# Kernel tuning notes

Hardware: AMD Instinct MI355X
Metric: run time of the kernel (lower is better)

## Reference

```python
import jax, jax.numpy as jnp
import numpy as np

N = 131072          # collocation points
NT, NX = 4, 8       # subdomain grid: 4 time segments x 8 space segments
S = NT * NX         # 32 subdomains
D = 2               # (t, x)
H = 32              # hidden width
OVERLAP = 0.3


def _make_subdomains():
    # t in [0,1] split into NT, x in [-1,1] split into NX
    t_edges = np.linspace(0.0, 1.0, NT + 1)
    x_edges = np.linspace(-1.0, 1.0, NX + 1)
    centers, widths, cmin, cmax = [], [], [], []
    for i in range(NT):
        for j in range(NX):
            lo = np.array([t_edges[i], x_edges[j]])
            hi = np.array([t_edges[i + 1], x_edges[j + 1]])
            centers.append((lo + hi) / 2)
            widths.append(hi - lo)
            cmin.append(lo)
            cmax.append(hi)
    f32 = lambda a: jnp.asarray(np.stack(a), dtype=jnp.float32)
    return f32(centers), f32(widths), f32(cmin), f32(cmax)


def setup_inputs() -> dict:
    key = jax.random.key(0)
    ks = jax.random.split(key, 12)
    # collocation points: t ~ U[0,1], x ~ U[-1,1]
    u = jax.random.uniform(ks[0], (N, D), dtype=jnp.float32)
    X = jnp.stack([u[:, 0], 2.0 * u[:, 1] - 1.0], axis=-1)
    centers, widths, core_min, core_max = _make_subdomains()
    overlap = jnp.full((S, D), OVERLAP, dtype=jnp.float32)
    g = lambda k, sh, fan: (jax.random.normal(k, sh, dtype=jnp.float32)
                            / np.sqrt(fan).astype(np.float32))
    return {
        "X": X,
        "centers": centers, "widths": widths,
        "core_min": core_min, "core_max": core_max, "overlap": overlap,
        "W1": g(ks[1], (S, D, H), D), "b1": jnp.zeros((S, H), jnp.float32),
        "W2": g(ks[2], (S, H, H), H), "b2": jnp.zeros((S, H), jnp.float32),
        "W3": g(ks[3], (S, H, H), H), "b3": jnp.zeros((S, H), jnp.float32),
        "Wout": g(ks[4], (S, H, 1), H), "bout": jnp.zeros((S, 1), jnp.float32),
        "scale": jnp.ones((1,), jnp.float32), "shift": jnp.zeros((1,), jnp.float32),
    }


def reference(X, centers, widths, core_min, core_max, overlap,
              W1, b1, W2, b2, W3, b3, Wout, bout, scale, shift):
    # --- window weights, all subdomains at once: (S, N) ---
    s = 4.0 / (2.0 * overlap * widths + 1e-8)            # (S, D)
    left = jax.nn.sigmoid(s[:, None] * (X[None] - core_min[:, None]))   # (S,N,D)
    right = jax.nn.sigmoid(s[:, None] * (core_max[:, None] - X[None]))  # (S,N,D)
    w = (left * right).prod(axis=-1)                     # (S, N)
    w = w / (w.sum(axis=0, keepdims=True) + 1e-8)

    # --- per-subdomain normalization + batched 3-hidden-layer tanh MLP ---
    xn = (X[None] - centers[:, None]) / widths[:, None] + 0.5           # (S,N,D)
    h = jnp.tanh(jnp.einsum('snd,sdh->snh', xn, W1) + b1[:, None])
    h = jnp.tanh(jnp.einsum('snh,shk->snk', h, W2) + b2[:, None])
    h = jnp.tanh(jnp.einsum('snh,shk->snk', h, W3) + b3[:, None])
    y = jnp.einsum('snh,sho->sno', h, Wout) + bout[:, None]             # (S,N,1)
    y = scale * y + shift                                # shared Unnorm

    out = jnp.sum(w[..., None] * y, axis=0)              # (N, 1)

    # --- hard BC constraint layer ---
    x = X[:, 1]
    t = X[:, 0]
    factor = jnp.tanh(x + 1.0) * jnp.tanh(x - 1.0) * jnp.tanh(t)
    out = -jnp.sin(jnp.pi * x)[:, None] + factor[:, None] * out
    return out
```

## Files before the change

### kernel.cpp

```cpp
#include <hip/hip_runtime.h>
#include <math.h>

typedef short    bf16x8 __attribute__((ext_vector_type(8)));
typedef float    f32x16 __attribute__((ext_vector_type(16)));
typedef float    f32x4  __attribute__((ext_vector_type(4)));
typedef unsigned int u32x4 __attribute__((ext_vector_type(4)));

#define SWZ(row) ((((row) >> 1) & 3) << 3)

__device__ __forceinline__ unsigned short f2bf(float f) {
    unsigned int u = __builtin_bit_cast(unsigned int, f);
    u = (u + 0x7FFFu + ((u >> 16) & 1u)) >> 16;
    return (unsigned short)u;
}
__device__ __forceinline__ unsigned int cvt_pk_bf16(float lo, float hi) {
    unsigned int r;
    asm("v_cvt_pk_bf16_f32 %0, %1, %2" : "=v"(r) : "v"(lo), "v"(hi));
    return r;
}
__device__ __forceinline__ float rcp_fast(float x) { return __builtin_amdgcn_rcpf(x); }

__device__ __forceinline__ float tanh_f(float z) {
    return fmaf(-2.0f, rcp_fast(__expf(2.0f * z) + 1.0f), 1.0f);
}
__device__ __forceinline__ unsigned int sx32(unsigned int v) {
    return (unsigned int)__shfl_xor((int)v, 32, 64);
}

__global__ __launch_bounds__(256) void fbpinn_main(
    const float* __restrict__ X,
    const float* __restrict__ centers,
    const float* __restrict__ widths,
    const float* __restrict__ core_min,
    const float* __restrict__ core_max,
    const float* __restrict__ overlap,
    const float* __restrict__ W1,
    const float* __restrict__ b1,
    const float* __restrict__ W2,
    const float* __restrict__ b2,
    const float* __restrict__ W3,
    const float* __restrict__ b3,
    const float* __restrict__ Wout,
    const float* __restrict__ bout,
    float* __restrict__ ws,
    int n_pts, int s_count)
{
    __shared__ __align__(16) unsigned short sW2t[4][1024];
    __shared__ __align__(16) unsigned short sW3t[4][1024];
    __shared__ __align__(16) float sW1f[4][64];
    __shared__ __align__(16) float sB1[4][32], sB2[4][32], sB3[4][32], sWo[4][32];
    __shared__ float sBout[4];

    const int tid  = threadIdx.x;
    const int wave = tid >> 6;
    const int lane = tid & 63;
    const int p    = lane & 31;
    const int hi   = lane >> 5;
    const int s_begin = blockIdx.y * s_count;

    int P = blockIdx.x * 128 + wave * 32 + p;
    if (P >= n_pts) P = n_pts - 1;

    const float t = X[2 * P + 0];
    const float x = X[2 * P + 1];

    float num = 0.0f, den = 0.0f;

    const int ef0 = (p << 5) + ((hi * 8)      ^ SWZ(p));
    const int ef1 = (p << 5) + ((16 + hi * 8) ^ SWZ(p));

    for (int c0 = 0; c0 < s_count; c0 += 4) {
        __syncthreads();
        {
            const float* W2s = W2 + (size_t)(s_begin + c0) * 1024;
            const float* W3s = W3 + (size_t)(s_begin + c0) * 1024;
            #pragma unroll
            for (int i = 0; i < 16; ++i) {
                int e = tid + (i << 8);
                int sl = e >> 10, r = e & 1023;
                int k = r >> 5, j = r & 31;
                int di = (j << 5) + (k ^ SWZ(j));
                sW2t[sl][di] = f2bf(W2s[e]);
                sW3t[sl][di] = f2bf(W3s[e]);
            }
            sW1f[tid >> 6][tid & 63] = W1[(size_t)(s_begin + c0) * 64 + tid];
            if (tid < 128) {
                int sl = tid >> 5, j = tid & 31;
                int g = (s_begin + c0 + sl) * 32 + j;
                sB1[sl][j] = b1[g];
                sB2[sl][j] = b2[g];
                sB3[sl][j] = b3[g];
                sWo[sl][j] = Wout[g];
            }
            if (tid < 4) sBout[tid] = bout[s_begin + c0 + tid];
        }
        __syncthreads();

        for (int si = 0; si < 4; ++si) {
            const int s = s_begin + c0 + si;

            float wid0 = widths[s * 2 + 0], wid1 = widths[s * 2 + 1];
            float sd0 = 4.0f * rcp_fast(fmaf(2.0f * overlap[s * 2 + 0], wid0, 1e-8f));
            float sd1 = 4.0f * rcp_fast(fmaf(2.0f * overlap[s * 2 + 1], wid1, 1e-8f));
            float z0 = sd0 * (t - core_min[s * 2 + 0]);
            float z1 = sd0 * (core_max[s * 2 + 0] - t);
            float z2 = sd1 * (x - core_min[s * 2 + 1]);
            float z3 = sd1 * (core_max[s * 2 + 1] - x);
            float w = rcp_fast(((1.0f + __expf(-z0)) * (1.0f + __expf(-z1)))
                             * ((1.0f + __expf(-z2)) * (1.0f + __expf(-z3))));
            float xn0 = (t - centers[s * 2 + 0]) * rcp_fast(wid0) + 0.5f;
            float xn1 = (x - centers[s * 2 + 1]) * rcp_fast(wid1) + 0.5f;

            unsigned int pk[8];

            {
                const f32x4* Wa4 = (const f32x4*)&sW1f[si][hi * 16];
                const f32x4* Wb4 = (const f32x4*)&sW1f[si][32 + hi * 16];
                const f32x4* Bv4 = (const f32x4*)&sB1[si][hi * 16];
                float Wa[16], Wb[16], Bv[16];
                #pragma unroll
                for (int i = 0; i < 4; ++i) {
                    f32x4 av = Wa4[i], bv = Wb4[i], cv = Bv4[i];
                    #pragma unroll
                    for (int q = 0; q < 4; ++q) {
                        Wa[4 * i + q] = av[q];
                        Wb[4 * i + q] = bv[q];
                        Bv[4 * i + q] = cv[q];
                    }
                }
                #pragma unroll
                for (int q = 0; q < 8; ++q) {
                    float a0 = fmaf(xn0, Wa[2 * q],     fmaf(xn1, Wb[2 * q],     Bv[2 * q]));
                    float a1 = fmaf(xn0, Wa[2 * q + 1], fmaf(xn1, Wb[2 * q + 1], Bv[2 * q + 1]));
                    pk[q] = cvt_pk_bf16(tanh_f(a0), tanh_f(a1));
                }
            }
            bf16x8 Bf0, Bf1;
            {
                unsigned int r0 = sx32(hi ? pk[0] : pk[4]);
                unsigned int r1 = sx32(hi ? pk[1] : pk[5]);
                unsigned int r2 = sx32(hi ? pk[2] : pk[6]);
                unsigned int r3 = sx32(hi ? pk[3] : pk[7]);
                u32x4 f1 = hi ? (u32x4){r0, r1, r2, r3} : (u32x4){pk[0], pk[1], pk[2], pk[3]};
                u32x4 f2 = hi ? (u32x4){pk[4], pk[5], pk[6], pk[7]} : (u32x4){r0, r1, r2, r3};
                Bf0 = __builtin_bit_cast(bf16x8, f1);
                Bf1 = __builtin_bit_cast(bf16x8, f2);
            }

            f32x16 acc;
            {
                bf16x8 A0 = *(bf16x8*)&sW2t[si][ef0];
                bf16x8 A1 = *(bf16x8*)&sW2t[si][ef1];
                #pragma unroll
                for (int i = 0; i < 4; ++i) {
                    f32x4 bv = *(const f32x4*)&sB2[si][8 * i + 4 * hi];
                    #pragma unroll
                    for (int q = 0; q < 4; ++q) acc[4 * i + q] = bv[q];
                }
                acc = __builtin_amdgcn_mfma_f32_32x32x16_bf16(A0, Bf0, acc, 0, 0, 0);
                acc = __builtin_amdgcn_mfma_f32_32x32x16_bf16(A1, Bf1, acc, 0, 0, 0);
            }
            #pragma unroll
            for (int q = 0; q < 8; ++q)
                pk[q] = cvt_pk_bf16(tanh_f(acc[2 * q]), tanh_f(acc[2 * q + 1]));
            {
                unsigned int r0 = sx32(hi ? pk[0] : pk[2]);
                unsigned int r1 = sx32(hi ? pk[1] : pk[3]);
                unsigned int r2 = sx32(hi ? pk[4] : pk[6]);
                unsigned int r3 = sx32(hi ? pk[5] : pk[7]);
                u32x4 f1 = hi ? (u32x4){r0, r1, pk[2], pk[3]} : (u32x4){pk[0], pk[1], r0, r1};
                u32x4 f2 = hi ? (u32x4){r2, r3, pk[6], pk[7]} : (u32x4){pk[4], pk[5], r2, r3};
                Bf0 = __builtin_bit_cast(bf16x8, f1);
                Bf1 = __builtin_bit_cast(bf16x8, f2);
            }

            {
                bf16x8 A0 = *(bf16x8*)&sW3t[si][ef0];
                bf16x8 A1 = *(bf16x8*)&sW3t[si][ef1];
                #pragma unroll
                for (int i = 0; i < 4; ++i) {
                    f32x4 bv = *(const f32x4*)&sB3[si][8 * i + 4 * hi];
                    #pragma unroll
                    for (int q = 0; q < 4; ++q) acc[4 * i + q] = bv[q];
                }
                acc = __builtin_amdgcn_mfma_f32_32x32x16_bf16(A0, Bf0, acc, 0, 0, 0);
                acc = __builtin_amdgcn_mfma_f32_32x32x16_bf16(A1, Bf1, acc, 0, 0, 0);
            }

            {
                float yp = 0.0f;
                #pragma unroll
                for (int i = 0; i < 4; ++i) {
                    f32x4 wv = *(const f32x4*)&sWo[si][8 * i + 4 * hi];
                    #pragma unroll
                    for (int q = 0; q < 4; ++q)
                        yp = fmaf(tanh_f(acc[4 * i + q]), wv[q], yp);
                }
                float y = yp + __shfl_xor(yp, 32, 64);
                y += sBout[si];
                num = fmaf(w, y, num);
                den += w;
            }
        }
    }

    if (hi == 0) {
        const int grp = blockIdx.y;
        ws[(size_t)(2 * grp)     * n_pts + P] = num;
        ws[(size_t)(2 * grp + 1) * n_pts + P] = den;
    }
}

__global__ __launch_bounds__(256) void fbpinn_combine(
    const float* __restrict__ X,
    const float* __restrict__ scale,
    const float* __restrict__ shift,
    const float* __restrict__ ws,
    float* __restrict__ out,
    int n_pts, int ngrp)
{
    const int P = blockIdx.x * 256 + threadIdx.x;
    if (P >= n_pts) return;
    float num = 0.0f, den = 0.0f;
    for (int g = 0; g < ngrp; ++g) {
        num += ws[(size_t)(2 * g)     * n_pts + P];
        den += ws[(size_t)(2 * g + 1) * n_pts + P];
    }
    const float sc = scale[0], sh = shift[0];
    float u = fmaf(sc, num, sh * den) / (den + 1e-8f);
    const float t = X[2 * P + 0];
    const float x = X[2 * P + 1];
    float fac = tanh_f(x + 1.0f) * tanh_f(x - 1.0f) * tanh_f(t);
    const float pi = 3.14159265358979323846f;
    out[P] = fmaf(fac, u, -__sinf(pi * x));
}

extern "C" void kernel_launch(void* const* d_in, const int* in_sizes, int n_in,
                              void* d_out, int out_size, void* d_ws, size_t ws_size,
                              hipStream_t stream) {
    const float* X        = (const float*)d_in[0];
    const float* centers  = (const float*)d_in[1];
    const float* widths   = (const float*)d_in[2];
    const float* core_min = (const float*)d_in[3];
    const float* core_max = (const float*)d_in[4];
    const float* overlap  = (const float*)d_in[5];
    const float* W1       = (const float*)d_in[6];
    const float* b1       = (const float*)d_in[7];
    const float* W2       = (const float*)d_in[8];
    const float* b2       = (const float*)d_in[9];
    const float* W3       = (const float*)d_in[10];
    const float* b3       = (const float*)d_in[11];
    const float* Wout     = (const float*)d_in[12];
    const float* bout     = (const float*)d_in[13];
    const float* scale    = (const float*)d_in[14];
    const float* shift    = (const float*)d_in[15];

    float* out = (float*)d_out;
    float* ws  = (float*)d_ws;
    const int n_pts = in_sizes[0] / 2;

    int ngrp = 8;
    while (ngrp > 1 && (size_t)2 * ngrp * n_pts * sizeof(float) > ws_size) ngrp >>= 1;
    const int s_count = 32 / ngrp;

    dim3 grid((n_pts + 127) / 128, ngrp);
    fbpinn_main<<<grid, 256, 0, stream>>>(
        X, centers, widths, core_min, core_max, overlap,
        W1, b1, W2, b2, W3, b3, Wout, bout,
        ws, n_pts, s_count);

    fbpinn_combine<<<(n_pts + 255) / 256, 256, 0, stream>>>(
        X, scale, shift, ws, out, n_pts, ngrp);
}
```

Baseline: 211.9 us.

## Fuse subdomain split and combine into a single kernel over all subdomains

Each block now loops over all 32 subdomains instead of splitting them across a grid y-dimension, and applies the normalization and hard boundary-condition epilogue directly. This removes the workspace partial-sum writes and reads and the second kernel launch. In exchange the grid shrinks eightfold, so each block runs eight serialized weight-staging phases with barriers, and there is less parallelism available to hide latency.

```diff
diff --git a/kernel.cpp b/kernel.cpp
--- a/kernel.cpp
+++ b/kernel.cpp
@@ -27,7 +27,7 @@
     return (unsigned int)__shfl_xor((int)v, 32, 64);
 }
 
-__global__ __launch_bounds__(256) void fbpinn_main(
+__global__ __launch_bounds__(256) void fbpinn_fused(
     const float* __restrict__ X,
     const float* __restrict__ centers,
     const float* __restrict__ widths,
@@ -42,8 +42,10 @@
     const float* __restrict__ b3,
     const float* __restrict__ Wout,
     const float* __restrict__ bout,
-    float* __restrict__ ws,
-    int n_pts, int s_count)
+    const float* __restrict__ scale,
+    const float* __restrict__ shift,
+    float* __restrict__ out,
+    int n_pts)
 {
     __shared__ __align__(16) unsigned short sW2t[4][1024];
     __shared__ __align__(16) unsigned short sW3t[4][1024];
@@ -56,24 +58,25 @@
     const int lane = tid & 63;
     const int p    = lane & 31;
     const int hi   = lane >> 5;
-    const int s_begin = blockIdx.y * s_count;
 
     int P = blockIdx.x * 128 + wave * 32 + p;
     if (P >= n_pts) P = n_pts - 1;
 
-    const float t = X[2 * P + 0];
-    const float x = X[2 * P + 1];
+    const float t  = X[2 * P + 0];
+    const float x  = X[2 * P + 1];
+    const float sc = scale[0];
+    const float sh = shift[0];
 
     float num = 0.0f, den = 0.0f;
 
     const int ef0 = (p << 5) + ((hi * 8)      ^ SWZ(p));
     const int ef1 = (p << 5) + ((16 + hi * 8) ^ SWZ(p));
 
-    for (int c0 = 0; c0 < s_count; c0 += 4) {
+    for (int c0 = 0; c0 < 32; c0 += 4) {
         __syncthreads();
         {
-            const float* W2s = W2 + (size_t)(s_begin + c0) * 1024;
-            const float* W3s = W3 + (size_t)(s_begin + c0) * 1024;
+            const float* W2s = W2 + (size_t)c0 * 1024;
+            const float* W3s = W3 + (size_t)c0 * 1024;
             #pragma unroll
             for (int i = 0; i < 16; ++i) {
                 int e = tid + (i << 8);
@@ -83,21 +86,21 @@
                 sW2t[sl][di] = f2bf(W2s[e]);
                 sW3t[sl][di] = f2bf(W3s[e]);
             }
-            sW1f[tid >> 6][tid & 63] = W1[(size_t)(s_begin + c0) * 64 + tid];
+            sW1f[tid >> 6][tid & 63] = W1[(size_t)c0 * 64 + tid];
             if (tid < 128) {
                 int sl = tid >> 5, j = tid & 31;
-                int g = (s_begin + c0 + sl) * 32 + j;
+                int g = (c0 + sl) * 32 + j;
                 sB1[sl][j] = b1[g];
                 sB2[sl][j] = b2[g];
                 sB3[sl][j] = b3[g];
                 sWo[sl][j] = Wout[g];
             }
-            if (tid < 4) sBout[tid] = bout[s_begin + c0 + tid];
+            if (tid < 4) sBout[tid] = bout[c0 + tid];
         }
         __syncthreads();
 
         for (int si = 0; si < 4; ++si) {
-            const int s = s_begin + c0 + si;
+            const int s = c0 + si;
 
             float wid0 = widths[s * 2 + 0], wid1 = widths[s * 2 + 1];
             float sd0 = 4.0f * rcp_fast(fmaf(2.0f * overlap[s * 2 + 0], wid0, 1e-8f));
@@ -205,34 +208,11 @@
     }
 
     if (hi == 0) {
-        const int grp = blockIdx.y;
-        ws[(size_t)(2 * grp)     * n_pts + P] = num;
-        ws[(size_t)(2 * grp + 1) * n_pts + P] = den;
+        float u = fmaf(sc, num, sh * den) / (den + 1e-8f);
+        float fac = tanh_f(x + 1.0f) * tanh_f(x - 1.0f) * tanh_f(t);
+        const float pi = 3.14159265358979323846f;
+        out[P] = fmaf(fac, u, -__sinf(pi * x));
     }
-}
-
-__global__ __launch_bounds__(256) void fbpinn_combine(
-    const float* __restrict__ X,
-    const float* __restrict__ scale,
-    const float* __restrict__ shift,
-    const float* __restrict__ ws,
-    float* __restrict__ out,
-    int n_pts, int ngrp)
-{
-    const int P = blockIdx.x * 256 + threadIdx.x;
-    if (P >= n_pts) return;
-    float num = 0.0f, den = 0.0f;
-    for (int g = 0; g < ngrp; ++g) {
-        num += ws[(size_t)(2 * g)     * n_pts + P];
-        den += ws[(size_t)(2 * g + 1) * n_pts + P];
-    }
-    const float sc = scale[0], sh = shift[0];
-    float u = fmaf(sc, num, sh * den) / (den + 1e-8f);
-    const float t = X[2 * P + 0];
-    const float x = X[2 * P + 1];
-    float fac = tanh_f(x + 1.0f) * tanh_f(x - 1.0f) * tanh_f(t);
-    const float pi = 3.14159265358979323846f;
-    out[P] = fmaf(fac, u, -__sinf(pi * x));
 }
 
 extern "C" void kernel_launch(void* const* d_in, const int* in_sizes, int n_in,
@@ -256,19 +236,11 @@
     const float* shift    = (const float*)d_in[15];
 
     float* out = (float*)d_out;
-    float* ws  = (float*)d_ws;
     const int n_pts = in_sizes[0] / 2;
 
-    int ngrp = 8;
-    while (ngrp > 1 && (size_t)2 * ngrp * n_pts * sizeof(float) > ws_size) ngrp >>= 1;
-    const int s_count = 32 / ngrp;
-
-    dim3 grid((n_pts + 127) / 128, ngrp);
-    fbpinn_main<<<grid, 256, 0, stream>>>(
+    const int grid = (n_pts + 127) / 128;
+    fbpinn_fused<<<grid, 256, 0, stream>>>(
         X, centers, widths, core_min, core_max, overlap,
-        W1, b1, W2, b2, W3, b3, Wout, bout,
-        ws, n_pts, s_count);
-
-    fbpinn_combine<<<(n_pts + 255) / 256, 256, 0, stream>>>(
-        X, scale, shift, ws, out, n_pts, ngrp);
-}
+        W1, b1, W2, b2, W3, b3, Wout, bout, scale, shift,
+        out, n_pts);
+}
```

New measurement: 230.5 us. +8.8%, slower.
